# Kernel tuning notes

Hardware: AMD Instinct MI355X
Metric: run time of the kernel (lower is better)

## Reference

```python
import jax, jax.numpy as jnp
import numpy as np

B, T, C, H = 2, 2048, 1024, 16
D = C // H  # head dim = 64


def setup_inputs() -> dict:
    key = jax.random.key(0)
    ks = jax.random.split(key, 5)
    s = 0.02
    return {
        "x": jax.random.normal(ks[0], (B, T, C), dtype=jnp.float32),
        "W_attn": jax.random.normal(ks[1], (C, 3 * C), dtype=jnp.float32) * s,
        "b_attn": jax.random.normal(ks[2], (3 * C,), dtype=jnp.float32) * s,
        "W_proj": jax.random.normal(ks[3], (C, C), dtype=jnp.float32) * s,
        "b_proj": jax.random.normal(ks[4], (C,), dtype=jnp.float32) * s,
    }


def reference(x, W_attn, b_attn, W_proj, b_proj):
    Bb, Tt, Cc = x.shape
    kqv = x @ W_attn + b_attn                     # [B,T,3C]
    q, k, v = jnp.split(kqv, 3, axis=2)           # each [B,T,C]
    # reshape to heads: [B,H,T,D]
    q = q.reshape(Bb, Tt, H, D).transpose(0, 2, 1, 3)
    k = k.reshape(Bb, Tt, H, D).transpose(0, 2, 1, 3)
    v = v.reshape(Bb, Tt, H, D).transpose(0, 2, 1, 3)
    scale = 1.0 / jnp.sqrt(jnp.float32(D))
    att = jnp.einsum('bhqd,bhkd->bhqk', q, k) * scale  # [B,H,T,T]
    causal = jnp.tril(jnp.ones((Tt, Tt), dtype=bool))
    att = jnp.where(causal[None, None], att, -jnp.inf)
    att = jax.nn.softmax(att, axis=-1)
    y = jnp.einsum('bhqk,bhkd->bhqd', att, v)      # [B,H,T,D]
    y = y.transpose(0, 2, 1, 3).reshape(Bb, Tt, Cc)
    return y @ W_proj + b_proj
```

## Files before the change

kernel.cpp:

```cpp
#include <hip/hip_runtime.h>
#include <hip/hip_bf16.h>
#include <math.h>

typedef __attribute__((ext_vector_type(4))) float f32x4;
typedef __attribute__((ext_vector_type(8))) short short8;
typedef __attribute__((ext_vector_type(4))) short short4v;

__device__ __forceinline__ short f2bf(float f) {
    union { __hip_bfloat16 h; short s; } u;
    u.h = __float2bfloat16(f);
    return u.s;
}

__global__ __launch_bounds__(256) void cvt_bf16(const float* __restrict__ in,
                                                short* __restrict__ out, int n) {
    int i = (blockIdx.x * 256 + threadIdx.x) * 8;
    if (i >= n) return;
    float4 a = *reinterpret_cast<const float4*>(in + i);
    float4 b = *reinterpret_cast<const float4*>(in + i + 4);
    short8 o;
    o[0] = f2bf(a.x); o[1] = f2bf(a.y); o[2] = f2bf(a.z); o[3] = f2bf(a.w);
    o[4] = f2bf(b.x); o[5] = f2bf(b.y); o[6] = f2bf(b.z); o[7] = f2bf(b.w);
    *reinterpret_cast<short8*>(out + i) = o;
}

__global__ __launch_bounds__(256) void transpose_w(const float* __restrict__ W,
                                                   short* __restrict__ Wt,
                                                   int K, int N) {
    __shared__ float tile[64][68];
    const int k0 = blockIdx.x * 64;
    const int n0 = blockIdx.y * 64;
    const int tid = threadIdx.x;
    #pragma unroll
    for (int i = 0; i < 4; ++i) {
        int c = tid + i * 256;
        int r = c >> 4;
        int col4 = (c & 15) * 4;
        float4 v = *reinterpret_cast<const float4*>(W + (size_t)(k0 + r) * N + n0 + col4);
        tile[r][col4 + 0] = v.x; tile[r][col4 + 1] = v.y;
        tile[r][col4 + 2] = v.z; tile[r][col4 + 3] = v.w;
    }
    __syncthreads();
    #pragma unroll
    for (int i = 0; i < 4; ++i) {
        int c = tid + i * 256;
        int r2 = c >> 4;
        int col4 = (c & 15) * 4;
        short4v o;
        #pragma unroll
        for (int j = 0; j < 4; ++j) o[j] = f2bf(tile[col4 + j][r2]);
        *reinterpret_cast<short4v*>(Wt + (size_t)(n0 + r2) * K + k0 + col4) = o;
    }
}

template<bool OUT_BF16>
__global__ __launch_bounds__(256) void gemm_bt(const short* __restrict__ A,
                                               const short* __restrict__ Bt,
                                               const float* __restrict__ bias,
                                               void* __restrict__ C,
                                               int M, int N, int K) {
    constexpr int BM = 128, BN = 128, BK = 64, LDP = BK + 8;
    __shared__ short As[BM * LDP];
    __shared__ short Bs[BN * LDP];
    const int tid = threadIdx.x;
    const int lane = tid & 63, wave = tid >> 6;
    const int bm = blockIdx.x * BM, bn = blockIdx.y * BN;
    const int wr = (wave >> 1) * 64, wc = (wave & 1) * 64;
    const int g = lane >> 4, l15 = lane & 15;

    f32x4 acc[4][4] = {};

    for (int k0 = 0; k0 < K; k0 += BK) {
        __syncthreads();
        #pragma unroll
        for (int i = 0; i < 4; ++i) {
            int c = tid + i * 256;
            int r = c >> 3;
            int col = (c & 7) * 8;
            *reinterpret_cast<short8*>(&As[r * LDP + col]) =
                *reinterpret_cast<const short8*>(A + (size_t)(bm + r) * K + k0 + col);
            *reinterpret_cast<short8*>(&Bs[r * LDP + col]) =
                *reinterpret_cast<const short8*>(Bt + (size_t)(bn + r) * K + k0 + col);
        }
        __syncthreads();
        #pragma unroll
        for (int kk = 0; kk < 2; ++kk) {
            short8 af[4], bfr[4];
            #pragma unroll
            for (int m = 0; m < 4; ++m)
                af[m] = *reinterpret_cast<const short8*>(&As[(wr + m * 16 + l15) * LDP + kk * 32 + g * 8]);
            #pragma unroll
            for (int n = 0; n < 4; ++n)
                bfr[n] = *reinterpret_cast<const short8*>(&Bs[(wc + n * 16 + l15) * LDP + kk * 32 + g * 8]);
            #pragma unroll
            for (int m = 0; m < 4; ++m)
                #pragma unroll
                for (int n = 0; n < 4; ++n)
                    acc[m][n] = __builtin_amdgcn_mfma_f32_16x16x32_bf16(af[m], bfr[n], acc[m][n], 0, 0, 0);
        }
    }

    #pragma unroll
    for (int m = 0; m < 4; ++m)
        #pragma unroll
        for (int n = 0; n < 4; ++n) {
            int gc = bn + wc + n * 16 + l15;
            float bv = bias[gc];
            #pragma unroll
            for (int r = 0; r < 4; ++r) {
                int gr = bm + wr + m * 16 + g * 4 + r;
                float v = acc[m][n][r] + bv;
                if (OUT_BF16)
                    reinterpret_cast<short*>(C)[(size_t)gr * N + gc] = f2bf(v);
                else
                    reinterpret_cast<float*>(C)[(size_t)gr * N + gc] = v;
            }
        }
}

__global__ __launch_bounds__(256) void attn_kernel(const short* __restrict__ kqv,
                                                   short* __restrict__ yatt) {
    constexpr int T = 2048, C = 1024, D = 64;
    constexpr int LDK = D + 8;
    __shared__ short Ks[64 * LDK];
    __shared__ short Vt[64 * LDK];
    __shared__ short Ps[4][32 * LDK];

    const int tid = threadIdx.x;
    const int lane = tid & 63, wave = tid >> 6;
    const int g = lane >> 4, l15 = lane & 15;
    const int qt = blockIdx.x;
    const int h = blockIdx.y;
    const int b = blockIdx.z;
    const int qs = qt * 128;
    const int q0w = qs + wave * 32;

    const size_t rowstride = 3 * C;
    const size_t baseQ = (size_t)b * T * rowstride + (size_t)h * D;
    const size_t baseK = baseQ + C;
    const size_t baseV = baseQ + 2 * C;

    short8 qf[2][2];
    #pragma unroll
    for (int m = 0; m < 2; ++m)
        #pragma unroll
        for (int kk = 0; kk < 2; ++kk)
            qf[m][kk] = *reinterpret_cast<const short8*>(
                kqv + baseQ + (size_t)(q0w + m * 16 + l15) * rowstride + kk * 32 + g * 8);

    f32x4 oacc[2][4] = {};
    float mstate[2][4], lstate[2][4];
    #pragma unroll
    for (int m = 0; m < 2; ++m)
        #pragma unroll
        for (int r = 0; r < 4; ++r) { mstate[m][r] = -INFINITY; lstate[m][r] = 0.f; }

    const int jmax = 2 * qt + 1;
    for (int j = 0; j <= jmax; ++j) {
        const int kvbase = j * 64;
        __syncthreads();
        #pragma unroll
        for (int i = 0; i < 2; ++i) {
            int c = tid + i * 256;
            int r = c >> 3;
            int col = (c & 7) * 8;
            short8 kv8 = *reinterpret_cast<const short8*>(
                kqv + baseK + (size_t)(kvbase + r) * rowstride + col);
            *reinterpret_cast<short8*>(&Ks[r * LDK + col]) = kv8;
            short8 vv8 = *reinterpret_cast<const short8*>(
                kqv + baseV + (size_t)(kvbase + r) * rowstride + col);
            #pragma unroll
            for (int jj = 0; jj < 8; ++jj) Vt[(col + jj) * LDK + r] = vv8[jj];
        }
        __syncthreads();

        f32x4 sacc[2][4] = {};
        #pragma unroll
        for (int kk = 0; kk < 2; ++kk) {
            short8 bfr[4];
            #pragma unroll
            for (int n = 0; n < 4; ++n)
                bfr[n] = *reinterpret_cast<const short8*>(&Ks[(n * 16 + l15) * LDK + kk * 32 + g * 8]);
            #pragma unroll
            for (int m = 0; m < 2; ++m)
                #pragma unroll
                for (int n = 0; n < 4; ++n)
                    sacc[m][n] = __builtin_amdgcn_mfma_f32_16x16x32_bf16(qf[m][kk], bfr[n], sacc[m][n], 0, 0, 0);
        }
        #pragma unroll
        for (int m = 0; m < 2; ++m)
            #pragma unroll
            for (int n = 0; n < 4; ++n) {
                f32x4 v = sacc[m][n];
                #pragma unroll
                for (int r = 0; r < 4; ++r) {
                    int row = q0w + m * 16 + g * 4 + r;
                    int col = kvbase + n * 16 + l15;
                    float s = v[r] * 0.125f;
                    v[r] = (col <= row) ? s : -INFINITY;
                }
                sacc[m][n] = v;
            }

        #pragma unroll
        for (int m = 0; m < 2; ++m)
            #pragma unroll
            for (int r = 0; r < 4; ++r) {
                float rm = fmaxf(fmaxf(sacc[m][0][r], sacc[m][1][r]),
                                 fmaxf(sacc[m][2][r], sacc[m][3][r]));
                #pragma unroll
                for (int w = 1; w < 16; w <<= 1) rm = fmaxf(rm, __shfl_xor(rm, w));
                float mn = fmaxf(mstate[m][r], rm);
                float corr = __expf(mstate[m][r] - mn);
                mstate[m][r] = mn;
                float ls = 0.f;
                #pragma unroll
                for (int n = 0; n < 4; ++n) {
                    float p = __expf(sacc[m][n][r] - mn);
                    ls += p;
                    Ps[wave][(m * 16 + g * 4 + r) * LDK + n * 16 + l15] = f2bf(p);
                }
                #pragma unroll
                for (int w = 1; w < 16; w <<= 1) ls += __shfl_xor(ls, w);
                lstate[m][r] = lstate[m][r] * corr + ls;
                #pragma unroll
                for (int nd = 0; nd < 4; ++nd) oacc[m][nd][r] *= corr;
            }
        __syncthreads();

        #pragma unroll
        for (int kk = 0; kk < 2; ++kk) {
            short8 vb[4];
            #pragma unroll
            for (int nd = 0; nd < 4; ++nd)
                vb[nd] = *reinterpret_cast<const short8*>(&Vt[(nd * 16 + l15) * LDK + kk * 32 + g * 8]);
            #pragma unroll
            for (int m = 0; m < 2; ++m) {
                short8 pa = *reinterpret_cast<const short8*>(&Ps[wave][(m * 16 + l15) * LDK + kk * 32 + g * 8]);
                #pragma unroll
                for (int nd = 0; nd < 4; ++nd)
                    oacc[m][nd] = __builtin_amdgcn_mfma_f32_16x16x32_bf16(pa, vb[nd], oacc[m][nd], 0, 0, 0);
            }
        }
    }

    #pragma unroll
    for (int m = 0; m < 2; ++m)
        #pragma unroll
        for (int nd = 0; nd < 4; ++nd)
            #pragma unroll
            for (int r = 0; r < 4; ++r) {
                int row = q0w + m * 16 + g * 4 + r;
                int col = nd * 16 + l15;
                float o = oacc[m][nd][r] / lstate[m][r];
                yatt[(size_t)b * T * C + (size_t)row * C + h * D + col] = f2bf(o);
            }
}

extern "C" void kernel_launch(void* const* d_in, const int* in_sizes, int n_in,
                              void* d_out, int out_size, void* d_ws, size_t ws_size,
                              hipStream_t stream) {
    constexpr int B = 2, T = 2048, C = 1024, H = 16;
    constexpr int M = B * T;
    constexpr int N1 = 3 * C;
    constexpr int K = C;

    const float* x      = (const float*)d_in[0];
    const float* W_attn = (const float*)d_in[1];
    const float* b_attn = (const float*)d_in[2];
    const float* W_proj = (const float*)d_in[3];
    const float* b_proj = (const float*)d_in[4];
    float* out = (float*)d_out;

    char* ws = (char*)d_ws;
    short* x_bf    = (short*)(ws);
    short* Wt_attn = (short*)(ws + 8388608);
    short* Wt_proj = (short*)(ws + 14680064);
    short* kqv     = (short*)(ws + 16777216);
    short* yatt    = (short*)(ws + 41943040);

    cvt_bf16<<<dim3(M * K / (256 * 8)), 256, 0, stream>>>(x, x_bf, M * K);
    transpose_w<<<dim3(K / 64, N1 / 64), 256, 0, stream>>>(W_attn, Wt_attn, K, N1);
    transpose_w<<<dim3(K / 64, C / 64), 256, 0, stream>>>(W_proj, Wt_proj, K, C);

    gemm_bt<true><<<dim3(M / 128, N1 / 128), 256, 0, stream>>>(x_bf, Wt_attn, b_attn, kqv, M, N1, K);
    attn_kernel<<<dim3(T / 128, H, B), 256, 0, stream>>>(kqv, yatt);
    gemm_bt<false><<<dim3(M / 128, C / 128), 256, 0, stream>>>(yatt, Wt_proj, b_proj, out, M, C, C);
}
```

Baseline: 224.1 us.

## Emit transposed V and prescaled Q from QKV GEMM, retile attention per wave

The QKV GEMM epilogue now writes Q (pre-multiplied by the softmax scale) and K into a packed [B*T,2048] buffer, and V transposed into a per-batch [C,T] buffer. This removes the scalar LDS transpose of V inside the attention loop. The attention kernel now uses 64-query tiles with 16 rows per wave and a 1D grid that reorders tiles so heavy and light causal tiles are interleaved. It also skips masked MFMA work on the diagonal block, applies the mask only on that block, and raises wave priority around the MFMA sections. The trade-offs are more blocks with twice the K/V reloads per query row, and scattered 8-byte stores for the transposed V.

```diff
diff --git a/kernel.cpp b/kernel.cpp
--- a/kernel.cpp
+++ b/kernel.cpp
@@ -53,11 +53,12 @@
     }
 }
 
-template<bool OUT_BF16>
+template<int MODE>
 __global__ __launch_bounds__(256) void gemm_bt(const short* __restrict__ A,
                                                const short* __restrict__ Bt,
                                                const float* __restrict__ bias,
                                                void* __restrict__ C,
+                                               short* __restrict__ vt,
                                                int M, int N, int K) {
     constexpr int BM = 128, BN = 128, BK = 64, LDP = BK + 8;
     __shared__ short As[BM * LDP];
@@ -106,161 +107,174 @@
         for (int n = 0; n < 4; ++n) {
             int gc = bn + wc + n * 16 + l15;
             float bv = bias[gc];
-            #pragma unroll
-            for (int r = 0; r < 4; ++r) {
-                int gr = bm + wr + m * 16 + g * 4 + r;
-                float v = acc[m][n][r] + bv;
-                if (OUT_BF16)
-                    reinterpret_cast<short*>(C)[(size_t)gr * N + gc] = f2bf(v);
-                else
-                    reinterpret_cast<float*>(C)[(size_t)gr * N + gc] = v;
-            }
-        }
-}
-
-__global__ __launch_bounds__(256) void attn_kernel(const short* __restrict__ kqv,
+            int gr0 = bm + wr + m * 16 + g * 4;
+            if (MODE == 0) {
+                #pragma unroll
+                for (int r = 0; r < 4; ++r)
+                    reinterpret_cast<float*>(C)[(size_t)(gr0 + r) * N + gc] = acc[m][n][r] + bv;
+            } else {
+                if (gc < 2048) {
+                    float sc = (gc < 1024) ? 0.125f : 1.0f;
+                    short* qkp = reinterpret_cast<short*>(C);
+                    #pragma unroll
+                    for (int r = 0; r < 4; ++r)
+                        qkp[(size_t)(gr0 + r) * 2048 + gc] = f2bf((acc[m][n][r] + bv) * sc);
+                } else {
+                    int cv = gc - 2048;
+                    int bb = gr0 >> 11;
+                    int t0 = gr0 & 2047;
+                    short4v o;
+                    #pragma unroll
+                    for (int r = 0; r < 4; ++r) o[r] = f2bf(acc[m][n][r] + bv);
+                    *reinterpret_cast<short4v*>(&vt[((size_t)(bb << 10) + cv) * 2048 + t0]) = o;
+                }
+            }
+        }
+}
+
+__global__ __launch_bounds__(256) void attn_kernel(const short* __restrict__ qk,
+                                                   const short* __restrict__ vt,
                                                    short* __restrict__ yatt) {
-    constexpr int T = 2048, C = 1024, D = 64;
-    constexpr int LDK = D + 8;
+    constexpr int T = 2048;
+    constexpr int LDK = 72;
     __shared__ short Ks[64 * LDK];
-    __shared__ short Vt[64 * LDK];
-    __shared__ short Ps[4][32 * LDK];
+    __shared__ short Vs[64 * LDK];
+    __shared__ short Ps[4][16 * LDK];
 
     const int tid = threadIdx.x;
     const int lane = tid & 63, wave = tid >> 6;
     const int g = lane >> 4, l15 = lane & 15;
-    const int qt = blockIdx.x;
-    const int h = blockIdx.y;
-    const int b = blockIdx.z;
-    const int qs = qt * 128;
-    const int q0w = qs + wave * 32;
-
-    const size_t rowstride = 3 * C;
-    const size_t baseQ = (size_t)b * T * rowstride + (size_t)h * D;
-    const size_t baseK = baseQ + C;
-    const size_t baseV = baseQ + 2 * C;
-
-    short8 qf[2][2];
-    #pragma unroll
-    for (int m = 0; m < 2; ++m)
-        #pragma unroll
-        for (int kk = 0; kk < 2; ++kk)
-            qf[m][kk] = *reinterpret_cast<const short8*>(
-                kqv + baseQ + (size_t)(q0w + m * 16 + l15) * rowstride + kk * 32 + g * 8);
-
-    f32x4 oacc[2][4] = {};
-    float mstate[2][4], lstate[2][4];
-    #pragma unroll
-    for (int m = 0; m < 2; ++m)
-        #pragma unroll
-        for (int r = 0; r < 4; ++r) { mstate[m][r] = -INFINITY; lstate[m][r] = 0.f; }
-
-    const int jmax = 2 * qt + 1;
-    for (int j = 0; j <= jmax; ++j) {
-        const int kvbase = j * 64;
+
+    const int i = blockIdx.x;
+    const int x = i & 7;
+    const int u = i >> 3;
+    const int g2 = u >> 5;
+    const int v = u & 31;
+    const int qt = (g2 & 1) ? v : 31 - v;
+    const int grp = x * 4 + g2;
+    const int h = grp & 15, b = grp >> 4;
+
+    const int qs = qt * 64;
+    const int q0w = qs + wave * 16;
+
+    const size_t baseQ = (size_t)b * T * 2048 + (size_t)h * 64;
+    const size_t baseK = baseQ + 1024;
+    const size_t vbase = ((size_t)b * 1024 + (size_t)h * 64) * 2048;
+
+    short8 qf[2];
+    #pragma unroll
+    for (int kk = 0; kk < 2; ++kk)
+        qf[kk] = *reinterpret_cast<const short8*>(
+            qk + baseQ + (size_t)(q0w + l15) * 2048 + kk * 32 + g * 8);
+
+    f32x4 oacc[4] = {};
+    float mst[4], lst[4];
+    #pragma unroll
+    for (int r = 0; r < 4; ++r) { mst[r] = -INFINITY; lst[r] = 0.f; }
+
+    for (int j = 0; j <= qt; ++j) {
+        const int kb = j * 64;
         __syncthreads();
         #pragma unroll
-        for (int i = 0; i < 2; ++i) {
-            int c = tid + i * 256;
+        for (int it = 0; it < 2; ++it) {
+            int c = tid + it * 256;
             int r = c >> 3;
             int col = (c & 7) * 8;
-            short8 kv8 = *reinterpret_cast<const short8*>(
-                kqv + baseK + (size_t)(kvbase + r) * rowstride + col);
-            *reinterpret_cast<short8*>(&Ks[r * LDK + col]) = kv8;
-            short8 vv8 = *reinterpret_cast<const short8*>(
-                kqv + baseV + (size_t)(kvbase + r) * rowstride + col);
-            #pragma unroll
-            for (int jj = 0; jj < 8; ++jj) Vt[(col + jj) * LDK + r] = vv8[jj];
+            *reinterpret_cast<short8*>(&Ks[r * LDK + col]) =
+                *reinterpret_cast<const short8*>(qk + baseK + (size_t)(kb + r) * 2048 + col);
+            *reinterpret_cast<short8*>(&Vs[r * LDK + col]) =
+                *reinterpret_cast<const short8*>(vt + vbase + (size_t)r * 2048 + kb + col);
         }
         __syncthreads();
 
-        f32x4 sacc[2][4] = {};
+        const bool diag = (j == qt);
+        const int nmax = diag ? (wave | 1) : 3;
+
+        f32x4 sacc[4] = {};
+        __builtin_amdgcn_s_setprio(1);
         #pragma unroll
         for (int kk = 0; kk < 2; ++kk) {
-            short8 bfr[4];
-            #pragma unroll
-            for (int n = 0; n < 4; ++n)
-                bfr[n] = *reinterpret_cast<const short8*>(&Ks[(n * 16 + l15) * LDK + kk * 32 + g * 8]);
-            #pragma unroll
-            for (int m = 0; m < 2; ++m)
-                #pragma unroll
-                for (int n = 0; n < 4; ++n)
-                    sacc[m][n] = __builtin_amdgcn_mfma_f32_16x16x32_bf16(qf[m][kk], bfr[n], sacc[m][n], 0, 0, 0);
-        }
-        #pragma unroll
-        for (int m = 0; m < 2; ++m)
             #pragma unroll
             for (int n = 0; n < 4; ++n) {
-                f32x4 v = sacc[m][n];
+                if (n > nmax) break;
+                short8 bfr = *reinterpret_cast<const short8*>(&Ks[(n * 16 + l15) * LDK + kk * 32 + g * 8]);
+                sacc[n] = __builtin_amdgcn_mfma_f32_16x16x32_bf16(qf[kk], bfr, sacc[n], 0, 0, 0);
+            }
+        }
+        __builtin_amdgcn_s_setprio(0);
+
+        if (diag) {
+            #pragma unroll
+            for (int n = 0; n < 4; ++n) {
+                if (n > nmax) break;
                 #pragma unroll
                 for (int r = 0; r < 4; ++r) {
-                    int row = q0w + m * 16 + g * 4 + r;
-                    int col = kvbase + n * 16 + l15;
-                    float s = v[r] * 0.125f;
-                    v[r] = (col <= row) ? s : -INFINITY;
+                    int row = q0w + g * 4 + r;
+                    int col = kb + n * 16 + l15;
+                    if (col > row) sacc[n][r] = -INFINITY;
                 }
-                sacc[m][n] = v;
-            }
-
-        #pragma unroll
-        for (int m = 0; m < 2; ++m)
-            #pragma unroll
-            for (int r = 0; r < 4; ++r) {
-                float rm = fmaxf(fmaxf(sacc[m][0][r], sacc[m][1][r]),
-                                 fmaxf(sacc[m][2][r], sacc[m][3][r]));
-                #pragma unroll
-                for (int w = 1; w < 16; w <<= 1) rm = fmaxf(rm, __shfl_xor(rm, w));
-                float mn = fmaxf(mstate[m][r], rm);
-                float corr = __expf(mstate[m][r] - mn);
-                mstate[m][r] = mn;
-                float ls = 0.f;
-                #pragma unroll
-                for (int n = 0; n < 4; ++n) {
-                    float p = __expf(sacc[m][n][r] - mn);
-                    ls += p;
-                    Ps[wave][(m * 16 + g * 4 + r) * LDK + n * 16 + l15] = f2bf(p);
-                }
-                #pragma unroll
-                for (int w = 1; w < 16; w <<= 1) ls += __shfl_xor(ls, w);
-                lstate[m][r] = lstate[m][r] * corr + ls;
-                #pragma unroll
-                for (int nd = 0; nd < 4; ++nd) oacc[m][nd][r] *= corr;
-            }
-        __syncthreads();
-
+            }
+        }
+
+        #pragma unroll
+        for (int r = 0; r < 4; ++r) {
+            float rm = sacc[0][r];
+            #pragma unroll
+            for (int n = 1; n < 4; ++n) {
+                if (n > nmax) break;
+                rm = fmaxf(rm, sacc[n][r]);
+            }
+            #pragma unroll
+            for (int w = 1; w < 16; w <<= 1) rm = fmaxf(rm, __shfl_xor(rm, w));
+            float mn = fmaxf(mst[r], rm);
+            float corr = __expf(mst[r] - mn);
+            mst[r] = mn;
+            float ls = 0.f;
+            #pragma unroll
+            for (int n = 0; n < 4; ++n) {
+                if (n > nmax) break;
+                float p = __expf(sacc[n][r] - mn);
+                ls += p;
+                Ps[wave][(g * 4 + r) * LDK + n * 16 + l15] = f2bf(p);
+            }
+            #pragma unroll
+            for (int w = 1; w < 16; w <<= 1) ls += __shfl_xor(ls, w);
+            lst[r] = lst[r] * corr + ls;
+            #pragma unroll
+            for (int nd = 0; nd < 4; ++nd) oacc[nd][r] *= corr;
+        }
+
+        const int kkmax = diag ? (wave >> 1) : 1;
+        __builtin_amdgcn_s_setprio(1);
         #pragma unroll
         for (int kk = 0; kk < 2; ++kk) {
-            short8 vb[4];
-            #pragma unroll
-            for (int nd = 0; nd < 4; ++nd)
-                vb[nd] = *reinterpret_cast<const short8*>(&Vt[(nd * 16 + l15) * LDK + kk * 32 + g * 8]);
-            #pragma unroll
-            for (int m = 0; m < 2; ++m) {
-                short8 pa = *reinterpret_cast<const short8*>(&Ps[wave][(m * 16 + l15) * LDK + kk * 32 + g * 8]);
-                #pragma unroll
-                for (int nd = 0; nd < 4; ++nd)
-                    oacc[m][nd] = __builtin_amdgcn_mfma_f32_16x16x32_bf16(pa, vb[nd], oacc[m][nd], 0, 0, 0);
-            }
-        }
-    }
-
-    #pragma unroll
-    for (int m = 0; m < 2; ++m)
-        #pragma unroll
-        for (int nd = 0; nd < 4; ++nd)
-            #pragma unroll
-            for (int r = 0; r < 4; ++r) {
-                int row = q0w + m * 16 + g * 4 + r;
-                int col = nd * 16 + l15;
-                float o = oacc[m][nd][r] / lstate[m][r];
-                yatt[(size_t)b * T * C + (size_t)row * C + h * D + col] = f2bf(o);
-            }
+            if (kk > kkmax) break;
+            short8 pa = *reinterpret_cast<const short8*>(&Ps[wave][l15 * LDK + kk * 32 + g * 8]);
+            #pragma unroll
+            for (int nd = 0; nd < 4; ++nd) {
+                short8 vb = *reinterpret_cast<const short8*>(&Vs[(nd * 16 + l15) * LDK + kk * 32 + g * 8]);
+                oacc[nd] = __builtin_amdgcn_mfma_f32_16x16x32_bf16(pa, vb, oacc[nd], 0, 0, 0);
+            }
+        }
+        __builtin_amdgcn_s_setprio(0);
+    }
+
+    #pragma unroll
+    for (int r = 0; r < 4; ++r) {
+        float rl = 1.0f / lst[r];
+        int row = q0w + g * 4 + r;
+        #pragma unroll
+        for (int nd = 0; nd < 4; ++nd) {
+            int col = nd * 16 + l15;
+            yatt[((size_t)b * T + row) * 1024 + h * 64 + col] = f2bf(oacc[nd][r] * rl);
+        }
+    }
 }
 
 extern "C" void kernel_launch(void* const* d_in, const int* in_sizes, int n_in,
                               void* d_out, int out_size, void* d_ws, size_t ws_size,
                               hipStream_t stream) {
-    constexpr int B = 2, T = 2048, C = 1024, H = 16;
+    constexpr int B = 2, T = 2048, C = 1024;
     constexpr int M = B * T;
     constexpr int N1 = 3 * C;
     constexpr int K = C;
@@ -276,14 +290,15 @@
     short* x_bf    = (short*)(ws);
     short* Wt_attn = (short*)(ws + 8388608);
     short* Wt_proj = (short*)(ws + 14680064);
-    short* kqv     = (short*)(ws + 16777216);
+    short* qk      = (short*)(ws + 16777216);
+    short* vt      = (short*)(ws + 33554432);
     short* yatt    = (short*)(ws + 41943040);
 
     cvt_bf16<<<dim3(M * K / (256 * 8)), 256, 0, stream>>>(x, x_bf, M * K);
     transpose_w<<<dim3(K / 64, N1 / 64), 256, 0, stream>>>(W_attn, Wt_attn, K, N1);
     transpose_w<<<dim3(K / 64, C / 64), 256, 0, stream>>>(W_proj, Wt_proj, K, C);
 
-    gemm_bt<true><<<dim3(M / 128, N1 / 128), 256, 0, stream>>>(x_bf, Wt_attn, b_attn, kqv, M, N1, K);
-    attn_kernel<<<dim3(T / 128, H, B), 256, 0, stream>>>(kqv, yatt);
-    gemm_bt<false><<<dim3(M / 128, C / 128), 256, 0, stream>>>(yatt, Wt_proj, b_proj, out, M, C, C);
-}
+    gemm_bt<1><<<dim3(M / 128, N1 / 128), 256, 0, stream>>>(x_bf, Wt_attn, b_attn, qk, vt, M, N1, K);
+    attn_kernel<<<dim3(1024), 256, 0, stream>>>(qk, vt, yatt);
+    gemm_bt<0><<<dim3(M / 128, C / 128), 256, 0, stream>>>(yatt, Wt_proj, b_proj, out, nullptr, M, C, C);
+}
```

Result: faster. 181.6 us (-19.0%).
